# Kernel optimization log

Hardware: AMD Instinct MI355X
Metric: run time of the kernel (lower is better)

Reference implementation:

```python
import jax, jax.numpy as jnp
import numpy as np

CAPSULE_WIDE = 8
CAPSULE_TALL = 4
FEAT = 784
FV = FEAT // CAPSULE_TALL  # 196
B = 32768


def _linear_params(key, out_dim, in_dim):
    kw, kb = jax.random.split(key)
    bound = 1.0 / np.sqrt(in_dim)
    W = jax.random.uniform(kw, (out_dim, in_dim), minval=-bound, maxval=bound, dtype=jnp.float32)
    b = jax.random.uniform(kb, (out_dim,), minval=-bound, maxval=bound, dtype=jnp.float32)
    return W, b


def setup_inputs() -> dict:
    key = jax.random.key(0)
    ks = jax.random.split(key, 7)
    x = jax.random.normal(ks[0], (B, FEAT), dtype=jnp.float32)
    W1, b1 = _linear_params(ks[1], FV, FV)
    W2, b2 = _linear_params(ks[2], FV, FV)
    W3, b3 = _linear_params(ks[3], FV, FV)
    Wd1, bd1 = _linear_params(ks[4], FEAT, FEAT)
    Wd2, bd2 = _linear_params(ks[5], FEAT, FEAT)
    Wo, bo = _linear_params(ks[6], 10, FEAT)
    return {"x": x, "W1": W1, "b1": b1, "W2": W2, "b2": b2, "W3": W3, "b3": b3,
            "Wd1": Wd1, "bd1": bd1, "Wd2": Wd2, "bd2": bd2, "Wo": Wo, "bo": bo}


def reference(x, W1, b1, W2, b2, W3, b3, Wd1, bd1, Wd2, bd2, Wo, bo):
    h = x  # [B, 784]
    for _ in range(CAPSULE_WIDE):
        v = h.reshape(h.shape[0], CAPSULE_TALL, FV)  # [B, T, FV]
        q = v @ W1.T + b1  # first_copy
        k = v @ W2.T + b2  # second_copy
        u = v @ W3.T + b3  # third_copy
        scores = jnp.einsum('btf,bsf->bts', q, k)  # [B, T, T], unscaled
        probs = jax.nn.softmax(scores, axis=-1)
        h = jnp.einsum('bts,bsf->btf', probs, u).reshape(h.shape[0], -1)
    dec = jax.nn.relu(h @ Wd1.T + bd1) @ Wd2.T + bd2  # output_decoder
    return jax.nn.softmax(dec @ Wo.T + bo, axis=-1)  # output_probability
```

## Files before the change

### kernel.cpp

```cpp
#include <hip/hip_runtime.h>
#include <math.h>

#define NT 256
#define NTC 512
typedef _Float16 f16;
typedef _Float16 half8 __attribute__((ext_vector_type(8)));
typedef _Float16 half4 __attribute__((ext_vector_type(4)));
typedef float floatx4 __attribute__((ext_vector_type(4)));

#define ROWSHR_ADD(v, N) \
  (v) += __int_as_float(__builtin_amdgcn_update_dpp(0, __float_as_int(v), 0x110 | (N), 0xF, 0xF, true))

#define WD1_OFF  0
#define WD2_OFF  1433600
#define WOT_OFF  2867200
#define D8_OFF   2917376
#define HBUF_OFF 2918400
#define D1_OFF   55347200
#define WPKH_OFF 55347200
#define WPKL_OFF 56185856
#define SSE      38464

__device__ inline void glds16(const void* g, void* l) {
  __builtin_amdgcn_global_load_lds((const __attribute__((address_space(1))) void*)g,
                                   (__attribute__((address_space(3))) void*)l, 16, 0, 0);
}

__global__ void k_prep_wd(const float* __restrict__ Wd, f16* __restrict__ W16) {
  int idx = blockIdx.x * NT + threadIdx.x;
  if (idx >= 896 * 800) return;
  int n = idx / 800, k = idx - n * 800;
  W16[idx] = (f16)((n < 784 && k < 784) ? Wd[n * 784 + k] : 0.f);
}

__global__ void k_prep_wo(const float* __restrict__ Wo, float* __restrict__ WoT) {
  int idx = blockIdx.x * NT + threadIdx.x;
  if (idx >= 784 * 16) return;
  int f = idx >> 4, n = idx & 15;
  WoT[idx] = (n < 10) ? Wo[n * 784 + f] : 0.f;
}

__global__ void k_mm(const float* __restrict__ A0, const float* __restrict__ B0,
                     float* __restrict__ C0, int ta, int tb, int sA, int sB, int sC) {
  const float* A = A0 + (size_t)blockIdx.y * sA;
  const float* B = B0 + (size_t)blockIdx.y * sB;
  float*       C = C0 + (size_t)blockIdx.y * sC;
  __shared__ float red[256];
  const int tid = threadIdx.x;
  const int o = blockIdx.x * 64 + (tid & 63);
  const int ks = tid >> 6;
  float s = 0.f;
  int p = 0, r = 0;
  if (o < 196 * 196) {
    p = o / 196; r = o - p * 196;
    const int c0 = ks * 49;
    #pragma unroll 7
    for (int c = c0; c < c0 + 49; ++c) {
      float a = ta ? A[c * 196 + p] : A[p * 196 + c];
      float b = tb ? B[r * 196 + c] : B[c * 196 + r];
      s += a * b;
    }
  }
  red[tid] = s;
  __syncthreads();
  if (tid < 64 && o < 196 * 196)
    C[p * 196 + r] = red[tid] + red[tid + 64] + red[tid + 128] + red[tid + 192];
}

__global__ void k_tr(const float* __restrict__ A0, float* __restrict__ C0, int sA, int sC) {
  const float* A = A0 + (size_t)blockIdx.y * sA;
  float*       C = C0 + (size_t)blockIdx.y * sC;
  int idx = blockIdx.x * NT + threadIdx.x;
  if (idx >= 196 * 196) return;
  int p = idx / 196, r = idx - p * 196;
  C[p * 196 + r] = A[r * 196 + p];
}

__global__ void k_prep_vec(const float* __restrict__ W2, const float* __restrict__ b1,
                           const float* __restrict__ b3,
                           const float* __restrict__ G, const float* __restrict__ Kbase,
                           float* __restrict__ gtab, float* __restrict__ d8out) {
  __shared__ float z[196], cbuf[8][196], dbuf[8][196], gbuf[8][196], d8s[196];
  const int tid = threadIdx.x;
  for (int t = tid; t < 196; t += NTC) {
    float s = 0.f;
    for (int f = 0; f < 196; ++f) s += b1[f] * W2[f * 196 + t];
    z[t] = s;
    cbuf[0][t] = b3[t];
  }
  for (int o = tid; o < 7 * 196; o += NTC) {
    int j = o / 196 + 1, t = o - (j - 1) * 196;
    const float* K = Kbase + (size_t)(j - 1) * SSE;
    float s = 0.f;
    for (int n = 0; n < 196; ++n) s += K[n * 196 + t] * b3[n];
    cbuf[j][t] = s;
  }
  __syncthreads();
  for (int o = tid; o < 8 * 196; o += NTC) {
    int i = o / 196, t = o - i * 196;
    float s = 0.f;
    for (int j = 0; j < i; ++j) s += cbuf[j][t];
    dbuf[i][t] = s;
    if (i == 7) d8s[t] = s + cbuf[7][t];
  }
  __syncthreads();
  for (int o = tid; o < 8 * 196; o += NTC) {
    int i = o / 196, t = o - i * 196;
    float s = z[t];
    for (int k = 0; k < 196; ++k) s += G[k * 196 + t] * dbuf[i][k];
    gbuf[i][t] = s;
  }
  __syncthreads();
  for (int o = tid; o < 8 * 196; o += NTC) {
    int i = o / 196, t = o - i * 196;
    float s;
    if (i == 0) {
      s = gbuf[0][t];
    } else {
      const float* K = Kbase + (size_t)(i - 1) * SSE;
      s = 0.f;
      for (int n = 0; n < 196; ++n) s += K[t * 196 + n] * gbuf[i][n];
    }
    gtab[i * 196 + t] = s;
  }
  for (int t = tid; t < 196; t += NTC) d8out[t] = d8s[t];
}

__global__ void k_prep_pack(const float* __restrict__ scr,
                            f16* __restrict__ Wph, f16* __restrict__ Wpl) {
  int idx = blockIdx.x * NT + threadIdx.x;
  if (idx >= 9 * 208 * 224) return;
  int s = idx / (208 * 224), rem = idx - s * (208 * 224);
  int n = rem / 224, k = rem - n * 224;
  float v = 0.f;
  if (k < 196) {
    if (n < 196) {
      const float* M = (s == 0) ? scr
                     : (s < 8 ? (scr + (size_t)(16 + s - 1) * SSE)
                              : (scr + (size_t)8 * SSE));
      v = M[k * 196 + n];
    } else if (n == 196 && s < 8) {
      v = scr[(size_t)23 * SSE + s * 196 + k];
    }
  }
  f16 hi = (f16)v;
  Wph[idx] = hi;
  Wpl[idx] = (f16)(v - (float)hi);
}

__global__ __launch_bounds__(NTC, 4)
void k_caps(const float* __restrict__ x,
            const f16* __restrict__ Wph, const f16* __restrict__ Wpl,
            const float* __restrict__ d8g,
            f16* __restrict__ hbuf) {
  __shared__ __align__(16) char smem[70656];
  f16*   vAhi = (f16*)smem;
  f16*   vAlo = (f16*)(smem + 29696);
  float* Sful = (float*)(smem + 59392);
  float* Rl   = (float*)(smem + 67584);
  float* Cm   = (float*)(smem + 69632);

  const int tid  = threadIdx.x;
  const int w    = tid >> 6;
  const int lane = tid & 63;
  const int l15  = lane & 15;
  const int quad = lane >> 4;
  const int e0   = blockIdx.x * 16;
  const bool haveJ1 = (w + 8) < 13;

  for (int idx = tid; idx < 16 * 196; idx += NTC) {
    int elem = idx / 196, g = idx - elem * 196;
    int t = g / 49, f = (g - t * 49) * 4;
    floatx4 v4 = *(const floatx4*)&x[(size_t)(e0 + elem) * 784 + g * 4];
    half4 h4, l4;
    #pragma unroll
    for (int q = 0; q < 4; ++q) {
      f16 h = (f16)v4[q];
      h4[q] = h;
      l4[q] = (f16)(v4[q] - (float)h);
    }
    int vo = (elem * 4 + t) * 232 + f;
    *(half4*)&vAhi[vo] = h4;
    *(half4*)&vAlo[vo] = l4;
  }
  for (int p = tid; p < 64 * 36; p += NTC) {
    int row = p / 36, c = 196 + (p - (p / 36) * 36);
    vAhi[row * 232 + c] = (f16)0;
    vAlo[row * 232 + c] = (f16)0;
  }
  for (int p = tid; p < 2048; p += NTC) Sful[p] = 0.f;
  __syncthreads();

  float vv0[4][4], vv1[4][4];
  {
    int c0 = w * 16 + l15;
    int c1 = 128 + w * 16 + l15;
    #pragma unroll
    for (int mt = 0; mt < 4; ++mt)
      #pragma unroll
      for (int s = 0; s < 4; ++s) {
        int ro = ((mt * 4 + quad) * 4 + s) * 232;
        vv0[mt][s] = (float)vAhi[ro + c0] + (float)vAlo[ro + c0];
        vv1[mt][s] = haveJ1 ? ((float)vAhi[ro + c1] + (float)vAlo[ro + c1]) : 0.f;
      }
  }

  #pragma unroll 1
  for (int i = 0; i < 8; ++i) {
    floatx4 acc0[4], acc1[4];
    #pragma unroll
    for (int mt = 0; mt < 4; ++mt) {
      acc0[mt] = (floatx4){0.f, 0.f, 0.f, 0.f};
      acc1[mt] = (floatx4){0.f, 0.f, 0.f, 0.f};
    }
    const int wb0 = ((i * 208 + w * 16 + l15) * 224) + quad * 8;
    const int wb1 = ((i * 208 + (w + 8) * 16 + l15) * 224) + quad * 8;
    #pragma unroll
    for (int ks = 0; ks < 7; ++ks) {
      half8 ah[4], al[4];
      #pragma unroll
      for (int mt = 0; mt < 4; ++mt) {
        int ao = (mt * 16 + l15) * 232 + ks * 32 + quad * 8;
        ah[mt] = *(const half8*)&vAhi[ao];
        al[mt] = *(const half8*)&vAlo[ao];
      }
      {
        half8 bh = *(const half8*)&Wph[wb0 + ks * 32];
        half8 bl = *(const half8*)&Wpl[wb0 + ks * 32];
        #pragma unroll
        for (int mt = 0; mt < 4; ++mt) {
          acc0[mt] = __builtin_amdgcn_mfma_f32_16x16x32_f16(ah[mt], bh, acc0[mt], 0, 0, 0);
          acc0[mt] = __builtin_amdgcn_mfma_f32_16x16x32_f16(ah[mt], bl, acc0[mt], 0, 0, 0);
          acc0[mt] = __builtin_amdgcn_mfma_f32_16x16x32_f16(al[mt], bh, acc0[mt], 0, 0, 0);
        }
      }
      if (haveJ1) {
        half8 bh = *(const half8*)&Wph[wb1 + ks * 32];
        half8 bl = *(const half8*)&Wpl[wb1 + ks * 32];
        #pragma unroll
        for (int mt = 0; mt < 4; ++mt) {
          acc1[mt] = __builtin_amdgcn_mfma_f32_16x16x32_f16(ah[mt], bh, acc1[mt], 0, 0, 0);
          acc1[mt] = __builtin_amdgcn_mfma_f32_16x16x32_f16(ah[mt], bl, acc1[mt], 0, 0, 0);
          acc1[mt] = __builtin_amdgcn_mfma_f32_16x16x32_f16(al[mt], bh, acc1[mt], 0, 0, 0);
        }
      }
    }
    #pragma unroll
    for (int mt = 0; mt < 4; ++mt) {
      float part[16];
      #pragma unroll
      for (int t = 0; t < 4; ++t)
        #pragma unroll
        for (int s = 0; s < 4; ++s)
          part[t * 4 + s] = acc0[mt][t] * vv0[mt][s] + acc1[mt][t] * vv1[mt][s];
      #pragma unroll
      for (int p = 0; p < 16; ++p) {
        ROWSHR_ADD(part[p], 8);
        ROWSHR_ADD(part[p], 4);
        ROWSHR_ADD(part[p], 2);
        ROWSHR_ADD(part[p], 1);
      }
      if (l15 == 0) {
        int elem = mt * 4 + quad;
        #pragma unroll
        for (int t = 0; t < 4; ++t)
          #pragma unroll
          for (int s = 0; s < 4; ++s)
            atomicAdd(&Sful[((i * 16 + elem) * 4 + t) * 4 + s], part[t * 4 + s]);
      }
    }
    if (w == 4 && l15 == 4) {
      #pragma unroll
      for (int mt = 0; mt < 4; ++mt)
        *(floatx4*)&Rl[i * 64 + mt * 16 + quad * 4] = acc1[mt];
    }
  }
  __syncthreads();

  if (tid < 16) {
    const int e = tid;
    float C[4][4] = {{1,0,0,0},{0,1,0,0},{0,0,1,0},{0,0,0,1}};
    #pragma unroll 1
    for (int i = 0; i < 8; ++i) {
      float M[4][4];
      #pragma unroll
      for (int a = 0; a < 4; ++a) {
        floatx4 mm = *(const floatx4*)&Sful[((i * 16 + e) * 4 + a) * 4];
        #pragma unroll
        for (int b = 0; b < 4; ++b) M[a][b] = mm[b];
      }
      floatx4 rv = *(const floatx4*)&Rl[i * 64 + e * 4];
      float T1[4][4], Cr[4];
      #pragma unroll
      for (int t = 0; t < 4; ++t)
        #pragma unroll
        for (int b = 0; b < 4; ++b)
          T1[t][b] = C[t][0]*M[0][b] + C[t][1]*M[1][b] + C[t][2]*M[2][b] + C[t][3]*M[3][b];
      #pragma unroll
      for (int s = 0; s < 4; ++s)
        Cr[s] = C[s][0]*rv[0] + C[s][1]*rv[1] + C[s][2]*rv[2] + C[s][3]*rv[3];
      float P[4][4];
      #pragma unroll
      for (int t = 0; t < 4; ++t) {
        float S[4];
        #pragma unroll
        for (int s = 0; s < 4; ++s)
          S[s] = T1[t][0]*C[s][0] + T1[t][1]*C[s][1] + T1[t][2]*C[s][2] + T1[t][3]*C[s][3] + Cr[s];
        float m = fmaxf(fmaxf(S[0], S[1]), fmaxf(S[2], S[3]));
        float e0_ = __expf(S[0] - m), e1 = __expf(S[1] - m);
        float e2 = __expf(S[2] - m), e3 = __expf(S[3] - m);
        float inv = 1.f / (e0_ + e1 + e2 + e3);
        P[t][0] = e0_ * inv; P[t][1] = e1 * inv; P[t][2] = e2 * inv; P[t][3] = e3 * inv;
      }
      float Cn[4][4];
      #pragma unroll
      for (int t = 0; t < 4; ++t)
        #pragma unroll
        for (int s = 0; s < 4; ++s)
          Cn[t][s] = P[t][0]*C[0][s] + P[t][1]*C[1][s] + P[t][2]*C[2][s] + P[t][3]*C[3][s];
      #pragma unroll
      for (int t = 0; t < 4; ++t)
        #pragma unroll
        for (int s = 0; s < 4; ++s) C[t][s] = Cn[t][s];
    }
    #pragma unroll
    for (int t = 0; t < 4; ++t)
      *(floatx4*)&Cm[e * 16 + t * 4] = (floatx4){C[t][0], C[t][1], C[t][2], C[t][3]};
  }
  __syncthreads();

  {
    floatx4 acu0[4], acu1[4];
    #pragma unroll
    for (int mt = 0; mt < 4; ++mt) {
      acu0[mt] = (floatx4){0.f, 0.f, 0.f, 0.f};
      acu1[mt] = (floatx4){0.f, 0.f, 0.f, 0.f};
    }
    const int wb0 = ((8 * 208 + w * 16 + l15) * 224) + quad * 8;
    const int wb1 = ((8 * 208 + (w + 8) * 16 + l15) * 224) + quad * 8;
    #pragma unroll
    for (int ks = 0; ks < 7; ++ks) {
      half8 ah[4], al[4];
      #pragma unroll
      for (int mt = 0; mt < 4; ++mt) {
        int ao = (mt * 16 + l15) * 232 + ks * 32 + quad * 8;
        ah[mt] = *(const half8*)&vAhi[ao];
        al[mt] = *(const half8*)&vAlo[ao];
      }
      {
        half8 bh = *(const half8*)&Wph[wb0 + ks * 32];
        half8 bl = *(const half8*)&Wpl[wb0 + ks * 32];
        #pragma unroll
        for (int mt = 0; mt < 4; ++mt) {
          acu0[mt] = __builtin_amdgcn_mfma_f32_16x16x32_f16(ah[mt], bh, acu0[mt], 0, 0, 0);
          acu0[mt] = __builtin_amdgcn_mfma_f32_16x16x32_f16(ah[mt], bl, acu0[mt], 0, 0, 0);
          acu0[mt] = __builtin_amdgcn_mfma_f32_16x16x32_f16(al[mt], bh, acu0[mt], 0, 0, 0);
        }
      }
      if (haveJ1) {
        half8 bh = *(const half8*)&Wph[wb1 + ks * 32];
        half8 bl = *(const half8*)&Wpl[wb1 + ks * 32];
        #pragma unroll
        for (int mt = 0; mt < 4; ++mt) {
          acu1[mt] = __builtin_amdgcn_mfma_f32_16x16x32_f16(ah[mt], bh, acu1[mt], 0, 0, 0);
          acu1[mt] = __builtin_amdgcn_mfma_f32_16x16x32_f16(ah[mt], bl, acu1[mt], 0, 0, 0);
          acu1[mt] = __builtin_amdgcn_mfma_f32_16x16x32_f16(al[mt], bh, acu1[mt], 0, 0, 0);
        }
      }
    }
    const int f0 = w * 16 + l15;
    const int f1 = 128 + w * 16 + l15;
    const bool doF1 = haveJ1 && (f1 < 196);
    float d80 = d8g[f0];
    float d81 = doF1 ? d8g[f1] : 0.f;
    #pragma unroll
    for (int mt = 0; mt < 4; ++mt) {
      int elem = mt * 4 + quad;
      floatx4 c0 = *(const floatx4*)&Cm[elem * 16 + 0];
      floatx4 c1 = *(const floatx4*)&Cm[elem * 16 + 4];
      floatx4 c2 = *(const floatx4*)&Cm[elem * 16 + 8];
      floatx4 c3 = *(const floatx4*)&Cm[elem * 16 + 12];
      {
        floatx4 u = acu0[mt];
        float h0 = c0[0]*u[0] + c0[1]*u[1] + c0[2]*u[2] + c0[3]*u[3] + d80;
        float h1 = c1[0]*u[0] + c1[1]*u[1] + c1[2]*u[2] + c1[3]*u[3] + d80;
        float h2 = c2[0]*u[0] + c2[1]*u[1] + c2[2]*u[2] + c2[3]*u[3] + d80;
        float h3 = c3[0]*u[0] + c3[1]*u[1] + c3[2]*u[2] + c3[3]*u[3] + d80;
        size_t base = (size_t)(e0 + elem) * 800;
        hbuf[base + 0 * 196 + f0] = (f16)h0;
        hbuf[base + 1 * 196 + f0] = (f16)h1;
        hbuf[base + 2 * 196 + f0] = (f16)h2;
        hbuf[base + 3 * 196 + f0] = (f16)h3;
      }
      if (doF1) {
        floatx4 u = acu1[mt];
        float h0 = c0[0]*u[0] + c0[1]*u[1] + c0[2]*u[2] + c0[3]*u[3] + d81;
        float h1 = c1[0]*u[0] + c1[1]*u[1] + c1[2]*u[2] + c1[3]*u[3] + d81;
        float h2 = c2[0]*u[0] + c2[1]*u[1] + c2[2]*u[2] + c2[3]*u[3] + d81;
        float h3 = c3[0]*u[0] + c3[1]*u[1] + c3[2]*u[2] + c3[3]*u[3] + d81;
        size_t base = (size_t)(e0 + elem) * 800;
        hbuf[base + 0 * 196 + f1] = (f16)h0;
        hbuf[base + 1 * 196 + f1] = (f16)h1;
        hbuf[base + 2 * 196 + f1] = (f16)h2;
        hbuf[base + 3 * 196 + f1] = (f16)h3;
      }
    }
  }
  for (int idx = tid; idx < 256; idx += NTC)
    hbuf[(size_t)(e0 + (idx >> 4)) * 800 + 784 + (idx & 15)] = (f16)0;
}

__global__ __launch_bounds__(NT, 2)
void k_dec(const f16* __restrict__ A, const f16* __restrict__ Bw,
           const float* __restrict__ bias, f16* __restrict__ C, int do_relu) {
  __shared__ __align__(16) f16 As[128 * 32];
  __shared__ __align__(16) f16 Bs[128 * 32];
  const int tid = threadIdx.x, w = tid >> 6, lane = tid & 63;
  const int l15 = lane & 15, quad = lane >> 4;
  const int m0 = blockIdx.x * 128, n0 = blockIdx.y * 128;
  const int wm = w & 1, wn = w >> 1;
  const int srow = lane >> 2, soff = (lane & 3) * 8;

  floatx4 acc[4][4];
  #pragma unroll
  for (int nt = 0; nt < 4; ++nt) {
    int col = n0 + wn * 64 + nt * 16 + l15;
    float bb = (col < 784) ? bias[col] : 0.f;
    #pragma unroll
    for (int mt = 0; mt < 4; ++mt) acc[mt][nt] = (floatx4){bb, bb, bb, bb};
  }

  for (int kk = 0; kk < 25; ++kk) {
    __syncthreads();
    #pragma unroll
    for (int i = 0; i < 2; ++i) {
      int r = w * 32 + i * 16;
      glds16(&A[(size_t)(m0 + r + srow) * 800 + kk * 32 + soff], &As[r * 32]);
      glds16(&Bw[(size_t)(n0 + r + srow) * 800 + kk * 32 + soff], &Bs[r * 32]);
    }
    __syncthreads();
    half8 af[4], bf[4];
    #pragma unroll
    for (int mt = 0; mt < 4; ++mt)
      af[mt] = *(const half8*)&As[(wm * 64 + mt * 16 + l15) * 32 + quad * 8];
    #pragma unroll
    for (int nt = 0; nt < 4; ++nt)
      bf[nt] = *(const half8*)&Bs[(wn * 64 + nt * 16 + l15) * 32 + quad * 8];
    #pragma unroll
    for (int mt = 0; mt < 4; ++mt)
      #pragma unroll
      for (int nt = 0; nt < 4; ++nt)
        acc[mt][nt] = __builtin_amdgcn_mfma_f32_16x16x32_f16(af[mt], bf[nt], acc[mt][nt], 0, 0, 0);
  }

  #pragma unroll
  for (int nt = 0; nt < 4; ++nt) {
    int gcol = n0 + wn * 64 + nt * 16 + l15;
    if (gcol < 800) {
      #pragma unroll
      for (int mt = 0; mt < 4; ++mt) {
        #pragma unroll
        for (int r = 0; r < 4; ++r) {
          int grow = m0 + wm * 64 + mt * 16 + quad * 4 + r;
          float v = acc[mt][nt][r];
          if (do_relu) v = fmaxf(v, 0.f);
          C[(size_t)grow * 800 + gcol] = (f16)v;
        }
      }
    }
  }
}

__global__ __launch_bounds__(NT, 4)
void k_logits(const f16* __restrict__ d2, const float* __restrict__ WoT,
              const float* __restrict__ bo, float* __restrict__ out) {
  __shared__ __align__(16) f16 ds[16 * 800];
  __shared__ float lg[160];
  const int tid = threadIdx.x;
  const size_t e0 = (size_t)blockIdx.x * 16;
  for (int i = tid; i < 16 * 98; i += NT) {
    int e = i / 98, c = (i - e * 98) * 8;
    *(half8*)&ds[e * 800 + c] = *(const half8*)&d2[(e0 + e) * 800 + c];
  }
  __syncthreads();
  {
    int e = tid >> 4, n = tid & 15;
    const f16* dp = &ds[e * 800];
    float s = 0.f;
    #pragma unroll 4
    for (int f = 0; f < 784; ++f) s += (float)dp[f] * WoT[f * 16 + n];
    if (n < 10) lg[e * 10 + n] = s + bo[n];
  }
  __syncthreads();
  if (tid < 16) {
    float l[10], m = -1e30f;
    #pragma unroll
    for (int n = 0; n < 10; ++n) { l[n] = lg[tid * 10 + n]; m = fmaxf(m, l[n]); }
    float sum = 0.f;
    #pragma unroll
    for (int n = 0; n < 10; ++n) { l[n] = __expf(l[n] - m); sum += l[n]; }
    float inv = 1.f / sum;
    #pragma unroll
    for (int n = 0; n < 10; ++n) out[(e0 + tid) * 10 + n] = l[n] * inv;
  }
}

extern "C" void kernel_launch(void* const* d_in, const int* in_sizes, int n_in,
                              void* d_out, int out_size, void* d_ws, size_t ws_size,
                              hipStream_t stream) {
  const float* x   = (const float*)d_in[0];
  const float* W1  = (const float*)d_in[1];
  const float* b1  = (const float*)d_in[2];
  const float* W2  = (const float*)d_in[3];
  const float* W3  = (const float*)d_in[5];
  const float* b3  = (const float*)d_in[6];
  const float* Wd1 = (const float*)d_in[7];
  const float* bd1 = (const float*)d_in[8];
  const float* Wd2 = (const float*)d_in[9];
  const float* bd2 = (const float*)d_in[10];
  const float* Wo  = (const float*)d_in[11];
  const float* bo  = (const float*)d_in[12];
  float* out = (float*)d_out;

  char* ws = (char*)d_ws;
  f16*   Wd1p  = (f16*)(ws + WD1_OFF);
  f16*   Wd2p  = (f16*)(ws + WD2_OFF);
  float* WoTws = (float*)(ws + WOT_OFF);
  float* d8ws  = (float*)(ws + D8_OFF);
  f16*   hbuf  = (f16*)(ws + HBUF_OFF);
  f16*   d1buf = (f16*)(ws + D1_OFF);
  f16*   Wph   = (f16*)(ws + WPKH_OFF);
  f16*   Wpl   = (f16*)(ws + WPKL_OFF);
  float* scr   = (float*)(ws + HBUF_OFF);

  const int GTR = (196 * 196 + NT - 1) / NT;
  const int GSK = (196 * 196 + 63) / 64;

  k_prep_wd<<<(896 * 800 + NT - 1) / NT, NT, 0, stream>>>(Wd1, Wd1p);
  k_prep_wd<<<(896 * 800 + NT - 1) / NT, NT, 0, stream>>>(Wd2, Wd2p);
  k_prep_wo<<<(784 * 16 + NT - 1) / NT, NT, 0, stream>>>(Wo, WoTws);

  k_tr<<<dim3(GTR, 1), NT, 0, stream>>>(W3, scr + (size_t)1 * SSE, 0, 0);
  k_mm<<<dim3(GSK, 1), NT, 0, stream>>>(W1, W2, scr, 1, 0, 0, 0, 0);
  k_mm<<<dim3(GSK, 1), NT, 0, stream>>>(scr + (size_t)1 * SSE, scr + (size_t)1 * SSE,
                                        scr + (size_t)2 * SSE, 0, 0, 0, 0, 0);
  k_mm<<<dim3(GSK, 2), NT, 0, stream>>>(scr + (size_t)2 * SSE, scr + (size_t)1 * SSE,
                                        scr + (size_t)3 * SSE, 0, 0, 0, SSE, SSE);
  k_mm<<<dim3(GSK, 4), NT, 0, stream>>>(scr + (size_t)4 * SSE, scr + (size_t)1 * SSE,
                                        scr + (size_t)5 * SSE, 0, 0, 0, SSE, SSE);
  k_mm<<<dim3(GSK, 7), NT, 0, stream>>>(scr + (size_t)1 * SSE, scr,
                                        scr + (size_t)9 * SSE, 0, 0, SSE, 0, SSE);
  k_tr<<<dim3(GTR, 7), NT, 0, stream>>>(scr + (size_t)1 * SSE, scr + (size_t)24 * SSE, SSE, SSE);
  k_mm<<<dim3(GSK, 7), NT, 0, stream>>>(scr + (size_t)9 * SSE, scr + (size_t)24 * SSE,
                                        scr + (size_t)16 * SSE, 0, 0, SSE, SSE, SSE);
  k_prep_vec<<<1, NTC, 0, stream>>>(W2, b1, b3, scr, scr + (size_t)1 * SSE,
                                    scr + (size_t)23 * SSE, d8ws);
  k_prep_pack<<<(9 * 208 * 224 + NT - 1) / NT, NT, 0, stream>>>(scr, Wph, Wpl);

  k_caps<<<32768 / 16, NTC, 0, stream>>>(x, Wph, Wpl, d8ws, hbuf);
  k_dec<<<dim3(32768 / 128, 7), NT, 0, stream>>>(hbuf, Wd1p, bd1, d1buf, 1);
  k_dec<<<dim3(32768 / 128, 7), NT, 0, stream>>>(d1buf, Wd2p, bd2, hbuf, 0);
  k_logits<<<32768 / 16, NT, 0, stream>>>(hbuf, WoTws, bo, out);
}
```

Measured before the change: 905.0 us.

## Merge transpose launches into prep kernels and parallelize vector prep across blocks

Replaces the separate transpose kernels with a fused k_prep_gq that computes W1^T W2 and copies W3 in one launch, and drops the second transpose by switching later matmuls and the pack step to transposed indexing. k_prep_vec is split across 8 blocks, one per capsule iteration, each recomputing its own power-series vector instead of a single 512-thread block doing all of them. The capsule kernel pads the Sful score buffer to a stride of 20 floats, likely to reduce LDS bank conflicts on atomics, and unrolls the iteration loop by 2. This trades fewer launches and more parallel setup for redundant per-block recomputation and some extra shared memory.

After: 858.4 us. 1.05x faster.

```diff
diff --git a/kernel.cpp b/kernel.cpp
--- a/kernel.cpp
+++ b/kernel.cpp
@@ -67,63 +67,79 @@
     C[p * 196 + r] = red[tid] + red[tid + 64] + red[tid + 128] + red[tid + 192];
 }
 
-__global__ void k_tr(const float* __restrict__ A0, float* __restrict__ C0, int sA, int sC) {
-  const float* A = A0 + (size_t)blockIdx.y * sA;
-  float*       C = C0 + (size_t)blockIdx.y * sC;
-  int idx = blockIdx.x * NT + threadIdx.x;
-  if (idx >= 196 * 196) return;
-  int p = idx / 196, r = idx - p * 196;
-  C[p * 196 + r] = A[r * 196 + p];
+__global__ void k_prep_gq(const float* __restrict__ W1, const float* __restrict__ W2,
+                          const float* __restrict__ W3, float* __restrict__ scr) {
+  if (blockIdx.x < 601) {
+    __shared__ float red[256];
+    const int tid = threadIdx.x;
+    const int o = blockIdx.x * 64 + (tid & 63);
+    const int ks = tid >> 6;
+    float s = 0.f;
+    int p = 0, r = 0;
+    if (o < 196 * 196) {
+      p = o / 196; r = o - p * 196;
+      const int c0 = ks * 49;
+      #pragma unroll 7
+      for (int c = c0; c < c0 + 49; ++c)
+        s += W1[c * 196 + p] * W2[c * 196 + r];
+    }
+    red[tid] = s;
+    __syncthreads();
+    if (tid < 64 && o < 196 * 196)
+      scr[p * 196 + r] = red[tid] + red[tid + 64] + red[tid + 128] + red[tid + 192];
+  } else {
+    int idx = (blockIdx.x - 601) * NT + threadIdx.x;
+    if (idx < 196 * 196) scr[(size_t)SSE + idx] = W3[idx];
+  }
 }
 
 __global__ void k_prep_vec(const float* __restrict__ W2, const float* __restrict__ b1,
                            const float* __restrict__ b3,
-                           const float* __restrict__ G, const float* __restrict__ Kbase,
+                           const float* __restrict__ G, const float* __restrict__ Qbase,
                            float* __restrict__ gtab, float* __restrict__ d8out) {
-  __shared__ float z[196], cbuf[8][196], dbuf[8][196], gbuf[8][196], d8s[196];
+  __shared__ float z[196], cj[196], d[196], tmp[196];
+  const int i = blockIdx.x;
   const int tid = threadIdx.x;
-  for (int t = tid; t < 196; t += NTC) {
+  const float* W3 = Qbase;
+  for (int t = tid; t < 196; t += NT) {
     float s = 0.f;
     for (int f = 0; f < 196; ++f) s += b1[f] * W2[f * 196 + t];
     z[t] = s;
-    cbuf[0][t] = b3[t];
-  }
-  for (int o = tid; o < 7 * 196; o += NTC) {
-    int j = o / 196 + 1, t = o - (j - 1) * 196;
-    const float* K = Kbase + (size_t)(j - 1) * SSE;
-    float s = 0.f;
-    for (int n = 0; n < 196; ++n) s += K[n * 196 + t] * b3[n];
-    cbuf[j][t] = s;
-  }
-  __syncthreads();
-  for (int o = tid; o < 8 * 196; o += NTC) {
-    int i = o / 196, t = o - i * 196;
-    float s = 0.f;
-    for (int j = 0; j < i; ++j) s += cbuf[j][t];
-    dbuf[i][t] = s;
-    if (i == 7) d8s[t] = s + cbuf[7][t];
-  }
-  __syncthreads();
-  for (int o = tid; o < 8 * 196; o += NTC) {
-    int i = o / 196, t = o - i * 196;
+    d[t] = 0.f;
+    cj[t] = b3[t];
+  }
+  __syncthreads();
+  for (int j = 0; j < i; ++j) {
+    for (int t = tid; t < 196; t += NT) {
+      float s = 0.f;
+      for (int c = 0; c < 196; ++c) s += W3[t * 196 + c] * cj[c];
+      tmp[t] = s;
+      d[t] += cj[t];
+    }
+    __syncthreads();
+    for (int t = tid; t < 196; t += NT) cj[t] = tmp[t];
+    __syncthreads();
+  }
+  if (i == 7) {
+    for (int t = tid; t < 196; t += NT) d8out[t] = d[t] + cj[t];
+  }
+  for (int t = tid; t < 196; t += NT) {
     float s = z[t];
-    for (int k = 0; k < 196; ++k) s += G[k * 196 + t] * dbuf[i][k];
-    gbuf[i][t] = s;
-  }
-  __syncthreads();
-  for (int o = tid; o < 8 * 196; o += NTC) {
-    int i = o / 196, t = o - i * 196;
+    for (int k = 0; k < 196; ++k) s += G[k * 196 + t] * d[k];
+    tmp[t] = s;
+  }
+  __syncthreads();
+  for (int t = tid; t < 196; t += NT) {
     float s;
     if (i == 0) {
-      s = gbuf[0][t];
+      s = tmp[t];
     } else {
-      const float* K = Kbase + (size_t)(i - 1) * SSE;
+      const float* Qi = Qbase + (size_t)(i - 1) * SSE;
       s = 0.f;
-      for (int n = 0; n < 196; ++n) s += K[t * 196 + n] * gbuf[i][n];
+      for (int n = 0; n < 196; ++n) s += Qi[n * 196 + t] * tmp[n];
     }
     gtab[i * 196 + t] = s;
   }
-  for (int t = tid; t < 196; t += NTC) d8out[t] = d8s[t];
 }
 
 __global__ void k_prep_pack(const float* __restrict__ scr,
@@ -135,10 +151,12 @@
   float v = 0.f;
   if (k < 196) {
     if (n < 196) {
-      const float* M = (s == 0) ? scr
-                     : (s < 8 ? (scr + (size_t)(16 + s - 1) * SSE)
-                              : (scr + (size_t)8 * SSE));
-      v = M[k * 196 + n];
+      if (s == 8) {
+        v = scr[(size_t)8 * SSE + n * 196 + k];
+      } else {
+        const float* M = (s == 0) ? scr : (scr + (size_t)(16 + s - 1) * SSE);
+        v = M[k * 196 + n];
+      }
     } else if (n == 196 && s < 8) {
       v = scr[(size_t)23 * SSE + s * 196 + k];
     }
@@ -153,12 +171,12 @@
             const f16* __restrict__ Wph, const f16* __restrict__ Wpl,
             const float* __restrict__ d8g,
             f16* __restrict__ hbuf) {
-  __shared__ __align__(16) char smem[70656];
+  __shared__ __align__(16) char smem[72704];
   f16*   vAhi = (f16*)smem;
   f16*   vAlo = (f16*)(smem + 29696);
   float* Sful = (float*)(smem + 59392);
-  float* Rl   = (float*)(smem + 67584);
-  float* Cm   = (float*)(smem + 69632);
+  float* Rl   = (float*)(smem + 69632);
+  float* Cm   = (float*)(smem + 71680);
 
   const int tid  = threadIdx.x;
   const int w    = tid >> 6;
@@ -188,7 +206,7 @@
     vAhi[row * 232 + c] = (f16)0;
     vAlo[row * 232 + c] = (f16)0;
   }
-  for (int p = tid; p < 2048; p += NTC) Sful[p] = 0.f;
+  for (int p = tid; p < 8 * 16 * 20; p += NTC) Sful[p] = 0.f;
   __syncthreads();
 
   float vv0[4][4], vv1[4][4];
@@ -205,7 +223,7 @@
       }
   }
 
-  #pragma unroll 1
+  #pragma unroll 2
   for (int i = 0; i < 8; ++i) {
     floatx4 acc0[4], acc1[4];
     #pragma unroll
@@ -266,7 +284,7 @@
         for (int t = 0; t < 4; ++t)
           #pragma unroll
           for (int s = 0; s < 4; ++s)
-            atomicAdd(&Sful[((i * 16 + elem) * 4 + t) * 4 + s], part[t * 4 + s]);
+            atomicAdd(&Sful[(i * 16 + elem) * 20 + t * 4 + s], part[t * 4 + s]);
       }
     }
     if (w == 4 && l15 == 4) {
@@ -285,7 +303,7 @@
       float M[4][4];
       #pragma unroll
       for (int a = 0; a < 4; ++a) {
-        floatx4 mm = *(const floatx4*)&Sful[((i * 16 + e) * 4 + a) * 4];
+        floatx4 mm = *(const floatx4*)&Sful[(i * 16 + e) * 20 + a * 4];
         #pragma unroll
         for (int b = 0; b < 4; ++b) M[a][b] = mm[b];
       }
@@ -533,28 +551,25 @@
   f16*   Wpl   = (f16*)(ws + WPKL_OFF);
   float* scr   = (float*)(ws + HBUF_OFF);
 
-  const int GTR = (196 * 196 + NT - 1) / NT;
   const int GSK = (196 * 196 + 63) / 64;
+  const int GCP = (196 * 196 + NT - 1) / NT;
 
   k_prep_wd<<<(896 * 800 + NT - 1) / NT, NT, 0, stream>>>(Wd1, Wd1p);
   k_prep_wd<<<(896 * 800 + NT - 1) / NT, NT, 0, stream>>>(Wd2, Wd2p);
   k_prep_wo<<<(784 * 16 + NT - 1) / NT, NT, 0, stream>>>(Wo, WoTws);
 
-  k_tr<<<dim3(GTR, 1), NT, 0, stream>>>(W3, scr + (size_t)1 * SSE, 0, 0);
-  k_mm<<<dim3(GSK, 1), NT, 0, stream>>>(W1, W2, scr, 1, 0, 0, 0, 0);
-  k_mm<<<dim3(GSK, 1), NT, 0, stream>>>(scr + (size_t)1 * SSE, scr + (size_t)1 * SSE,
-                                        scr + (size_t)2 * SSE, 0, 0, 0, 0, 0);
+  k_prep_gq<<<GSK + GCP, NT, 0, stream>>>(W1, W2, W3, scr);
+  k_mm<<<dim3(GSK, 1), NT, 0, stream>>>(W3, W3, scr + (size_t)2 * SSE, 0, 0, 0, 0, 0);
   k_mm<<<dim3(GSK, 2), NT, 0, stream>>>(scr + (size_t)2 * SSE, scr + (size_t)1 * SSE,
                                         scr + (size_t)3 * SSE, 0, 0, 0, SSE, SSE);
   k_mm<<<dim3(GSK, 4), NT, 0, stream>>>(scr + (size_t)4 * SSE, scr + (size_t)1 * SSE,
                                         scr + (size_t)5 * SSE, 0, 0, 0, SSE, SSE);
   k_mm<<<dim3(GSK, 7), NT, 0, stream>>>(scr + (size_t)1 * SSE, scr,
-                                        scr + (size_t)9 * SSE, 0, 0, SSE, 0, SSE);
-  k_tr<<<dim3(GTR, 7), NT, 0, stream>>>(scr + (size_t)1 * SSE, scr + (size_t)24 * SSE, SSE, SSE);
-  k_mm<<<dim3(GSK, 7), NT, 0, stream>>>(scr + (size_t)9 * SSE, scr + (size_t)24 * SSE,
+                                        scr + (size_t)9 * SSE, 1, 0, SSE, 0, SSE);
+  k_mm<<<dim3(GSK, 7), NT, 0, stream>>>(scr + (size_t)9 * SSE, scr + (size_t)1 * SSE,
                                         scr + (size_t)16 * SSE, 0, 0, SSE, SSE, SSE);
-  k_prep_vec<<<1, NTC, 0, stream>>>(W2, b1, b3, scr, scr + (size_t)1 * SSE,
-                                    scr + (size_t)23 * SSE, d8ws);
+  k_prep_vec<<<8, NT, 0, stream>>>(W2, b1, b3, scr, scr + (size_t)1 * SSE,
+                                   scr + (size_t)23 * SSE, d8ws);
   k_prep_pack<<<(9 * 208 * 224 + NT - 1) / NT, NT, 0, stream>>>(scr, Wph, Wpl);
 
   k_caps<<<32768 / 16, NTC, 0, stream>>>(x, Wph, Wpl, d8ws, hbuf);
```

## Fuse weight-precompute chain into one cooperative kernel with grid syncs

Applied to the files above, without the earlier changes.

Replaces the sequence of small matmul, transpose, vector-prep and pack kernels with a single cooperative kernel that runs phases separated by grid.sync. Independent matrix-power products are grouped into the same phase so more work runs in parallel, and the serial single-block vector computation is spread across blocks. This is meant to cut launch overhead and the serialization of the long dependent prep chain. It adds cooperative-launch constraints: all 1024 blocks must be co-resident, and the dependency ordering between phases has to be correct.

Result: slower. 1.506 ms (+66.4%).

```diff
diff --git a/kernel.cpp b/kernel.cpp
--- a/kernel.cpp
+++ b/kernel.cpp
@@ -1,5 +1,8 @@
 #include <hip/hip_runtime.h>
+#include <hip/hip_cooperative_groups.h>
 #include <math.h>
+
+namespace cg = cooperative_groups;
 
 #define NT 256
 #define NTC 512
@@ -40,112 +43,169 @@
   WoT[idx] = (n < 10) ? Wo[n * 784 + f] : 0.f;
 }
 
-__global__ void k_mm(const float* __restrict__ A0, const float* __restrict__ B0,
-                     float* __restrict__ C0, int ta, int tb, int sA, int sB, int sC) {
-  const float* A = A0 + (size_t)blockIdx.y * sA;
-  const float* B = B0 + (size_t)blockIdx.y * sB;
-  float*       C = C0 + (size_t)blockIdx.y * sC;
-  __shared__ float red[256];
-  const int tid = threadIdx.x;
-  const int o = blockIdx.x * 64 + (tid & 63);
-  const int ks = tid >> 6;
+__device__ inline void mm_unit(const float* __restrict__ A, const float* __restrict__ B,
+                               float* __restrict__ C, int ta, int u, float* red, int tid) {
+  __syncthreads();
+  int o = u * 64 + (tid & 63);
+  int ks = tid >> 6;
   float s = 0.f;
   int p = 0, r = 0;
-  if (o < 196 * 196) {
+  if (o < 38416) {
     p = o / 196; r = o - p * 196;
     const int c0 = ks * 49;
     #pragma unroll 7
     for (int c = c0; c < c0 + 49; ++c) {
       float a = ta ? A[c * 196 + p] : A[p * 196 + c];
-      float b = tb ? B[r * 196 + c] : B[c * 196 + r];
-      s += a * b;
+      s += a * B[c * 196 + r];
     }
   }
   red[tid] = s;
   __syncthreads();
-  if (tid < 64 && o < 196 * 196)
+  if (tid < 64 && o < 38416)
     C[p * 196 + r] = red[tid] + red[tid + 64] + red[tid + 128] + red[tid + 192];
 }
 
-__global__ void k_tr(const float* __restrict__ A0, float* __restrict__ C0, int sA, int sC) {
-  const float* A = A0 + (size_t)blockIdx.y * sA;
-  float*       C = C0 + (size_t)blockIdx.y * sC;
-  int idx = blockIdx.x * NT + threadIdx.x;
-  if (idx >= 196 * 196) return;
-  int p = idx / 196, r = idx - p * 196;
-  C[p * 196 + r] = A[r * 196 + p];
-}
-
-__global__ void k_prep_vec(const float* __restrict__ W2, const float* __restrict__ b1,
-                           const float* __restrict__ b3,
-                           const float* __restrict__ G, const float* __restrict__ Kbase,
-                           float* __restrict__ gtab, float* __restrict__ d8out) {
-  __shared__ float z[196], cbuf[8][196], dbuf[8][196], gbuf[8][196], d8s[196];
+#define SL(i) (scr + (size_t)(i) * SSE)
+#define PU 601
+
+__global__ __launch_bounds__(NT, 4)
+void k_prep_all(const float* __restrict__ W1, const float* __restrict__ W2,
+                const float* __restrict__ W3, const float* __restrict__ b1,
+                const float* __restrict__ b3,
+                float* __restrict__ scr, float* __restrict__ d8out,
+                f16* __restrict__ Wph, f16* __restrict__ Wpl) {
+  __shared__ float red[256];
+  __shared__ float sc[196], sd[196], st[196];
   const int tid = threadIdx.x;
-  for (int t = tid; t < 196; t += NTC) {
-    float s = 0.f;
-    for (int f = 0; f < 196; ++f) s += b1[f] * W2[f * 196 + t];
-    z[t] = s;
-    cbuf[0][t] = b3[t];
-  }
-  for (int o = tid; o < 7 * 196; o += NTC) {
-    int j = o / 196 + 1, t = o - (j - 1) * 196;
-    const float* K = Kbase + (size_t)(j - 1) * SSE;
-    float s = 0.f;
-    for (int n = 0; n < 196; ++n) s += K[n * 196 + t] * b3[n];
-    cbuf[j][t] = s;
-  }
-  __syncthreads();
-  for (int o = tid; o < 8 * 196; o += NTC) {
-    int i = o / 196, t = o - i * 196;
-    float s = 0.f;
-    for (int j = 0; j < i; ++j) s += cbuf[j][t];
-    dbuf[i][t] = s;
-    if (i == 7) d8s[t] = s + cbuf[7][t];
-  }
-  __syncthreads();
-  for (int o = tid; o < 8 * 196; o += NTC) {
-    int i = o / 196, t = o - i * 196;
-    float s = z[t];
-    for (int k = 0; k < 196; ++k) s += G[k * 196 + t] * dbuf[i][k];
-    gbuf[i][t] = s;
-  }
-  __syncthreads();
-  for (int o = tid; o < 8 * 196; o += NTC) {
-    int i = o / 196, t = o - i * 196;
-    float s;
-    if (i == 0) {
-      s = gbuf[0][t];
+  cg::grid_group grid = cg::this_grid();
+
+  float* G    = scr;
+  float* gtab = scr + (size_t)23 * SSE;
+  float* zg   = gtab + 1600;
+  float* dtab = gtab + 1800;
+  float* gbuf = gtab + 3400;
+
+  for (int t = blockIdx.x; t < 2 * PU + 152; t += gridDim.x) {
+    if (t < PU) {
+      mm_unit(W1, W2, G, 1, t, red, tid);
+    } else if (t < 2 * PU) {
+      mm_unit(W3, W3, SL(2), 0, t - PU, red, tid);
+    } else if (t < 2 * PU + 151) {
+      int idx = (t - 2 * PU) * NT + tid;
+      if (idx < 38416) SL(1)[idx] = W3[idx];
     } else {
-      const float* K = Kbase + (size_t)(i - 1) * SSE;
-      s = 0.f;
-      for (int n = 0; n < 196; ++n) s += K[t * 196 + n] * gbuf[i][n];
-    }
-    gtab[i * 196 + t] = s;
-  }
-  for (int t = tid; t < 196; t += NTC) d8out[t] = d8s[t];
-}
-
-__global__ void k_prep_pack(const float* __restrict__ scr,
-                            f16* __restrict__ Wph, f16* __restrict__ Wpl) {
-  int idx = blockIdx.x * NT + threadIdx.x;
-  if (idx >= 9 * 208 * 224) return;
-  int s = idx / (208 * 224), rem = idx - s * (208 * 224);
-  int n = rem / 224, k = rem - n * 224;
-  float v = 0.f;
-  if (k < 196) {
-    if (n < 196) {
-      const float* M = (s == 0) ? scr
-                     : (s < 8 ? (scr + (size_t)(16 + s - 1) * SSE)
-                              : (scr + (size_t)8 * SSE));
-      v = M[k * 196 + n];
-    } else if (n == 196 && s < 8) {
-      v = scr[(size_t)23 * SSE + s * 196 + k];
-    }
-  }
-  f16 hi = (f16)v;
-  Wph[idx] = hi;
-  Wpl[idx] = (f16)(v - (float)hi);
+      for (int q = tid; q < 196; q += NT) {
+        float s = 0.f;
+        for (int f = 0; f < 196; ++f) s += b1[f] * W2[f * 196 + q];
+        zg[q] = s;
+      }
+      for (int q = tid; q < 196; q += NT) { sc[q] = b3[q]; sd[q] = 0.f; dtab[q] = 0.f; }
+      __syncthreads();
+      for (int j = 0; j < 7; ++j) {
+        for (int q = tid; q < 196; q += NT) {
+          float s = 0.f;
+          for (int c = 0; c < 196; ++c) s += W3[q * 196 + c] * sc[c];
+          st[q] = s;
+          sd[q] += sc[q];
+          dtab[(j + 1) * 196 + q] = sd[q];
+        }
+        __syncthreads();
+        for (int q = tid; q < 196; q += NT) sc[q] = st[q];
+        __syncthreads();
+      }
+      for (int q = tid; q < 196; q += NT) d8out[q] = sd[q] + sc[q];
+    }
+  }
+  grid.sync();
+
+  for (int t = blockIdx.x; t < 4 * PU + 8; t += gridDim.x) {
+    if (t < PU)          mm_unit(SL(2), W3,    SL(3),  0, t,          red, tid);
+    else if (t < 2 * PU) mm_unit(SL(2), SL(2), SL(4),  0, t - PU,     red, tid);
+    else if (t < 3 * PU) mm_unit(W3,    G,     SL(9),  1, t - 2 * PU, red, tid);
+    else if (t < 4 * PU) mm_unit(SL(2), G,     SL(10), 1, t - 3 * PU, red, tid);
+    else {
+      int i = t - 4 * PU;
+      for (int q = tid; q < 196; q += NT) {
+        float s = zg[q];
+        for (int k = 0; k < 196; ++k) s += G[k * 196 + q] * dtab[i * 196 + k];
+        gbuf[i * 196 + q] = s;
+      }
+    }
+  }
+  grid.sync();
+
+  for (int t = blockIdx.x; t < 8 * PU + 3; t += gridDim.x) {
+    if (t < PU)          mm_unit(SL(4),  W3,    SL(5),  0, t,          red, tid);
+    else if (t < 2 * PU) mm_unit(SL(4),  SL(2), SL(6),  0, t - PU,     red, tid);
+    else if (t < 3 * PU) mm_unit(SL(4),  SL(3), SL(7),  0, t - 2 * PU, red, tid);
+    else if (t < 4 * PU) mm_unit(SL(4),  SL(4), SL(8),  0, t - 3 * PU, red, tid);
+    else if (t < 5 * PU) mm_unit(SL(3),  G,     SL(11), 1, t - 4 * PU, red, tid);
+    else if (t < 6 * PU) mm_unit(SL(4),  G,     SL(12), 1, t - 5 * PU, red, tid);
+    else if (t < 7 * PU) mm_unit(SL(9),  W3,    SL(16), 0, t - 6 * PU, red, tid);
+    else if (t < 8 * PU) mm_unit(SL(10), SL(2), SL(17), 0, t - 7 * PU, red, tid);
+    else {
+      int i = t - 8 * PU;
+      for (int q = tid; q < 196; q += NT) {
+        float s;
+        if (i == 0) s = gbuf[q];
+        else {
+          const float* Qi = SL(i);
+          s = 0.f;
+          for (int n = 0; n < 196; ++n) s += Qi[n * 196 + q] * gbuf[i * 196 + n];
+        }
+        gtab[i * 196 + q] = s;
+      }
+    }
+  }
+  grid.sync();
+
+  for (int t = blockIdx.x; t < 5 * PU + 5; t += gridDim.x) {
+    if (t < PU)          mm_unit(SL(5),  G,     SL(13), 1, t,          red, tid);
+    else if (t < 2 * PU) mm_unit(SL(6),  G,     SL(14), 1, t - PU,     red, tid);
+    else if (t < 3 * PU) mm_unit(SL(7),  G,     SL(15), 1, t - 2 * PU, red, tid);
+    else if (t < 4 * PU) mm_unit(SL(11), SL(3), SL(18), 0, t - 3 * PU, red, tid);
+    else if (t < 5 * PU) mm_unit(SL(12), SL(4), SL(19), 0, t - 4 * PU, red, tid);
+    else {
+      int i = t - 5 * PU + 3;
+      const float* Qi = SL(i);
+      for (int q = tid; q < 196; q += NT) {
+        float s = 0.f;
+        for (int n = 0; n < 196; ++n) s += Qi[n * 196 + q] * gbuf[i * 196 + n];
+        gtab[i * 196 + q] = s;
+      }
+    }
+  }
+  grid.sync();
+
+  for (int t = blockIdx.x; t < 3 * PU; t += gridDim.x) {
+    if (t < PU)          mm_unit(SL(13), SL(5), SL(20), 0, t,          red, tid);
+    else if (t < 2 * PU) mm_unit(SL(14), SL(6), SL(21), 0, t - PU,     red, tid);
+    else                 mm_unit(SL(15), SL(7), SL(22), 0, t - 2 * PU, red, tid);
+  }
+  grid.sync();
+
+  for (int t = blockIdx.x; t < 1638; t += gridDim.x) {
+    int idx = t * NT + tid;
+    if (idx < 9 * 208 * 224) {
+      int s = idx / (208 * 224), rem = idx - s * (208 * 224);
+      int n = rem / 224, k = rem - n * 224;
+      float v = 0.f;
+      if (k < 196) {
+        if (n < 196) {
+          if (s == 8) v = SL(8)[n * 196 + k];
+          else {
+            const float* M = (s == 0) ? scr : SL(16 + s - 1);
+            v = M[k * 196 + n];
+          }
+        } else if (n == 196 && s < 8) {
+          v = gtab[s * 196 + k];
+        }
+      }
+      f16 hi = (f16)v;
+      Wph[idx] = hi;
+      Wpl[idx] = (f16)(v - (float)hi);
+    }
+  }
 }
 
 __global__ __launch_bounds__(NTC, 4)
@@ -533,29 +593,13 @@
   f16*   Wpl   = (f16*)(ws + WPKL_OFF);
   float* scr   = (float*)(ws + HBUF_OFF);
 
-  const int GTR = (196 * 196 + NT - 1) / NT;
-  const int GSK = (196 * 196 + 63) / 64;
-
   k_prep_wd<<<(896 * 800 + NT - 1) / NT, NT, 0, stream>>>(Wd1, Wd1p);
   k_prep_wd<<<(896 * 800 + NT - 1) / NT, NT, 0, stream>>>(Wd2, Wd2p);
   k_prep_wo<<<(784 * 16 + NT - 1) / NT, NT, 0, stream>>>(Wo, WoTws);
 
-  k_tr<<<dim3(GTR, 1), NT, 0, stream>>>(W3, scr + (size_t)1 * SSE, 0, 0);
-  k_mm<<<dim3(GSK, 1), NT, 0, stream>>>(W1, W2, scr, 1, 0, 0, 0, 0);
-  k_mm<<<dim3(GSK, 1), NT, 0, stream>>>(scr + (size_t)1 * SSE, scr + (size_t)1 * SSE,
-                                        scr + (size_t)2 * SSE, 0, 0, 0, 0, 0);
-  k_mm<<<dim3(GSK, 2), NT, 0, stream>>>(scr + (size_t)2 * SSE, scr + (size_t)1 * SSE,
-                                        scr + (size_t)3 * SSE, 0, 0, 0, SSE, SSE);
-  k_mm<<<dim3(GSK, 4), NT, 0, stream>>>(scr + (size_t)4 * SSE, scr + (size_t)1 * SSE,
-                                        scr + (size_t)5 * SSE, 0, 0, 0, SSE, SSE);
-  k_mm<<<dim3(GSK, 7), NT, 0, stream>>>(scr + (size_t)1 * SSE, scr,
-                                        scr + (size_t)9 * SSE, 0, 0, SSE, 0, SSE);
-  k_tr<<<dim3(GTR, 7), NT, 0, stream>>>(scr + (size_t)1 * SSE, scr + (size_t)24 * SSE, SSE, SSE);
-  k_mm<<<dim3(GSK, 7), NT, 0, stream>>>(scr + (size_t)9 * SSE, scr + (size_t)24 * SSE,
-                                        scr + (size_t)16 * SSE, 0, 0, SSE, SSE, SSE);
-  k_prep_vec<<<1, NTC, 0, stream>>>(W2, b1, b3, scr, scr + (size_t)1 * SSE,
-                                    scr + (size_t)23 * SSE, d8ws);
-  k_prep_pack<<<(9 * 208 * 224 + NT - 1) / NT, NT, 0, stream>>>(scr, Wph, Wpl);
+  void* kargs[] = {(void*)&W1, (void*)&W2, (void*)&W3, (void*)&b1, (void*)&b3,
+                   (void*)&scr, (void*)&d8ws, (void*)&Wph, (void*)&Wpl};
+  hipLaunchCooperativeKernel((void*)k_prep_all, dim3(1024), dim3(NT), kargs, 0, stream);
 
   k_caps<<<32768 / 16, NTC, 0, stream>>>(x, Wph, Wpl, d8ws, hbuf);
   k_dec<<<dim3(32768 / 128, 7), NT, 0, stream>>>(hbuf, Wd1p, bd1, d1buf, 1);
```
